# Performance work log

Measured on AMD Instinct MI355X. Metric: run time of the kernel, lower is better.

The kernel has to match this reference:

```python
import jax, jax.numpy as jnp
import numpy as np

B, N1, N2, D = 8, 2048, 2048, 512


def setup_inputs() -> dict:
    key = jax.random.key(0)
    k1, k2, k3 = jax.random.split(key, 3)
    matrix_1 = jax.random.normal(k1, (B, N1, D), dtype=jnp.float32)
    matrix_2 = jax.random.normal(k2, (B, N2, D), dtype=jnp.float32)
    # Linear similarity with combination 'x,y': weight over concat([x, y]) -> size 2*D
    weight = jax.random.normal(k3, (2 * D,), dtype=jnp.float32) * (1.0 / np.sqrt(2 * D))
    bias = jnp.zeros((1,), dtype=jnp.float32)
    return {"matrix_1": matrix_1, "matrix_2": matrix_2, "weight": weight, "bias": bias}


def reference(matrix_1, matrix_2, weight, bias):
    # Faithful to MatrixAttention + default Linear similarity:
    # sim[b,i,j] = dot(weight, concat(matrix_1[b,i], matrix_2[b,j])) + bias
    # The original tiles both matrices to (B, N1, N2, D); mathematically this
    # factors into two projections plus a broadcast add (same math, no tiling).
    d = matrix_1.shape[-1]
    w1, w2 = weight[:d], weight[d:]
    s1 = jnp.einsum('bnd,d->bn', matrix_1, w1)  # (B, N1)
    s2 = jnp.einsum('bmd,d->bm', matrix_2, w2)  # (B, N2)
    return s1[:, :, None] + s2[:, None, :] + bias[0]  # (B, N1, N2)
```

## Files before the change

kernel.cpp:

```cpp
#include <hip/hip_runtime.h>


#define DDIM 512
#define BB   8
#define NN   2048
#define ROWS_PER_MAT (BB * NN)

__global__ __launch_bounds__(256) void dot_kernel(const float* __restrict__ m1,
                                                  const float* __restrict__ m2,
                                                  const float* __restrict__ w,
                                                  float* __restrict__ s) {
    int wave = (int)((blockIdx.x * blockDim.x + threadIdx.x) >> 6);
    int lane = threadIdx.x & 63;

    const float* src;
    const float* wp;
    int row;
    if (wave < ROWS_PER_MAT) {
        src = m1; wp = w;        row = wave;
    } else {
        src = m2; wp = w + DDIM; row = wave - ROWS_PER_MAT;
    }

    const float4* rp = reinterpret_cast<const float4*>(src + (size_t)row * DDIM);
    const float4* wv = reinterpret_cast<const float4*>(wp);

    float4 a0 = rp[lane];
    float4 b0 = wv[lane];
    float4 a1 = rp[lane + 64];
    float4 b1 = wv[lane + 64];

    float acc = a0.x * b0.x + a0.y * b0.y + a0.z * b0.z + a0.w * b0.w
              + a1.x * b1.x + a1.y * b1.y + a1.z * b1.z + a1.w * b1.w;

    #pragma unroll
    for (int off = 32; off > 0; off >>= 1)
        acc += __shfl_down(acc, off, 64);

    if (lane == 0) s[wave] = acc;
}

__global__ __launch_bounds__(256) void add_kernel(const float* __restrict__ s1,
                                                  const float* __restrict__ s2,
                                                  const float* __restrict__ bias,
                                                  float4* __restrict__ out) {
    const size_t total4 = (size_t)BB * NN * (NN / 4);
    const float bval = bias[0];
    const float4* s2v = reinterpret_cast<const float4*>(s2);

    for (size_t i = (size_t)blockIdx.x * blockDim.x + threadIdx.x;
         i < total4;
         i += (size_t)gridDim.x * blockDim.x) {
        int m4    = (int)(i & (NN / 4 - 1));
        size_t t  = i >> 9;
        int n     = (int)(t & (NN - 1));
        int b     = (int)(t >> 11);

        float v1 = s1[b * NN + n] + bval;
        float4 v2 = s2v[b * (NN / 4) + m4];
        out[i] = make_float4(v2.x + v1, v2.y + v1, v2.z + v1, v2.w + v1);
    }
}

extern "C" void kernel_launch(void* const* d_in, const int* in_sizes, int n_in,
                              void* d_out, int out_size, void* d_ws, size_t ws_size,
                              hipStream_t stream) {
    const float* m1   = (const float*)d_in[0];
    const float* m2   = (const float*)d_in[1];
    const float* w    = (const float*)d_in[2];
    const float* bias = (const float*)d_in[3];
    float* out = (float*)d_out;

    float* s  = (float*)d_ws;
    float* s1 = s;
    float* s2 = s + ROWS_PER_MAT;

    dot_kernel<<<(2 * ROWS_PER_MAT) / 4, 256, 0, stream>>>(m1, m2, w, s);

    add_kernel<<<2048, 256, 0, stream>>>(s1, s2, bias, (float4*)out);
}
```

Before: 37.77 us.

## Fuse matrix_1 projection into broadcast-add kernel and use nontemporal loads/stores

The first kernel now projects only matrix_2 into the workspace. A new fused kernel has each wave compute one matrix_1 row projection and then write that row's full 2048-wide output line directly from s2. This removes the separate s1 workspace round trip and the grid-stride add kernel's per-element index math. Nontemporal loads for the input rows and nontemporal stores for the output are meant to keep the large streamed data from polluting cache. The trade-off is that each fused wave serializes its dot product before a long store loop, which could reduce memory-level parallelism.

```diff
diff --git a/kernel.cpp b/kernel.cpp
--- a/kernel.cpp
+++ b/kernel.cpp
@@ -4,61 +4,58 @@
 #define DDIM 512
 #define BB   8
 #define NN   2048
-#define ROWS_PER_MAT (BB * NN)
+#define ROWS (BB * NN)
 
-__global__ __launch_bounds__(256) void dot_kernel(const float* __restrict__ m1,
-                                                  const float* __restrict__ m2,
-                                                  const float* __restrict__ w,
-                                                  float* __restrict__ s) {
+typedef float f32x4 __attribute__((ext_vector_type(4)));
+
+__device__ __forceinline__ float dot_row_wave(const f32x4* __restrict__ rp,
+                                              const f32x4* __restrict__ wv,
+                                              int lane) {
+    f32x4 a0 = __builtin_nontemporal_load(rp + lane);
+    f32x4 b0 = wv[lane];
+    f32x4 a1 = __builtin_nontemporal_load(rp + lane + 64);
+    f32x4 b1 = wv[lane + 64];
+    float acc = a0.x * b0.x + a0.y * b0.y + a0.z * b0.z + a0.w * b0.w
+              + a1.x * b1.x + a1.y * b1.y + a1.z * b1.z + a1.w * b1.w;
+    #pragma unroll
+    for (int off = 1; off < 64; off <<= 1)
+        acc += __shfl_xor(acc, off, 64);
+    return acc;
+}
+
+__global__ __launch_bounds__(256) void dot2_kernel(const float* __restrict__ m2,
+                                                   const float* __restrict__ w,
+                                                   float* __restrict__ s2) {
     int wave = (int)((blockIdx.x * blockDim.x + threadIdx.x) >> 6);
     int lane = threadIdx.x & 63;
+    const f32x4* rp = reinterpret_cast<const f32x4*>(m2 + (size_t)wave * DDIM);
+    const f32x4* wv = reinterpret_cast<const f32x4*>(w + DDIM);
+    float acc = dot_row_wave(rp, wv, lane);
+    if (lane == 0) s2[wave] = acc;
+}
 
-    const float* src;
-    const float* wp;
-    int row;
-    if (wave < ROWS_PER_MAT) {
-        src = m1; wp = w;        row = wave;
-    } else {
-        src = m2; wp = w + DDIM; row = wave - ROWS_PER_MAT;
-    }
+__global__ __launch_bounds__(256) void fused_kernel(const float* __restrict__ m1,
+                                                    const float* __restrict__ w,
+                                                    const float* __restrict__ s2,
+                                                    const float* __restrict__ bias,
+                                                    float* __restrict__ out) {
+    int wave = (int)((blockIdx.x * blockDim.x + threadIdx.x) >> 6);
+    int lane = threadIdx.x & 63;
+    int b = wave >> 11;
 
-    const float4* rp = reinterpret_cast<const float4*>(src + (size_t)row * DDIM);
-    const float4* wv = reinterpret_cast<const float4*>(wp);
+    const f32x4* rp = reinterpret_cast<const f32x4*>(m1 + (size_t)wave * DDIM);
+    const f32x4* wv = reinterpret_cast<const f32x4*>(w);
+    float s1 = dot_row_wave(rp, wv, lane);
+    float v1 = s1 + bias[0];
 
-    float4 a0 = rp[lane];
-    float4 b0 = wv[lane];
-    float4 a1 = rp[lane + 64];
-    float4 b1 = wv[lane + 64];
-
-    float acc = a0.x * b0.x + a0.y * b0.y + a0.z * b0.z + a0.w * b0.w
-              + a1.x * b1.x + a1.y * b1.y + a1.z * b1.z + a1.w * b1.w;
+    const f32x4* s2v = reinterpret_cast<const f32x4*>(s2 + (size_t)b * NN);
+    f32x4* op = reinterpret_cast<f32x4*>(out + (size_t)wave * NN);
 
     #pragma unroll
-    for (int off = 32; off > 0; off >>= 1)
-        acc += __shfl_down(acc, off, 64);
-
-    if (lane == 0) s[wave] = acc;
-}
-
-__global__ __launch_bounds__(256) void add_kernel(const float* __restrict__ s1,
-                                                  const float* __restrict__ s2,
-                                                  const float* __restrict__ bias,
-                                                  float4* __restrict__ out) {
-    const size_t total4 = (size_t)BB * NN * (NN / 4);
-    const float bval = bias[0];
-    const float4* s2v = reinterpret_cast<const float4*>(s2);
-
-    for (size_t i = (size_t)blockIdx.x * blockDim.x + threadIdx.x;
-         i < total4;
-         i += (size_t)gridDim.x * blockDim.x) {
-        int m4    = (int)(i & (NN / 4 - 1));
-        size_t t  = i >> 9;
-        int n     = (int)(t & (NN - 1));
-        int b     = (int)(t >> 11);
-
-        float v1 = s1[b * NN + n] + bval;
-        float4 v2 = s2v[b * (NN / 4) + m4];
-        out[i] = make_float4(v2.x + v1, v2.y + v1, v2.z + v1, v2.w + v1);
+    for (int k = 0; k < 8; ++k) {
+        f32x4 v2 = s2v[lane + 64 * k];
+        f32x4 r  = v2 + v1;
+        __builtin_nontemporal_store(r, op + lane + 64 * k);
     }
 }
 
@@ -70,12 +67,8 @@
     const float* w    = (const float*)d_in[2];
     const float* bias = (const float*)d_in[3];
     float* out = (float*)d_out;
+    float* s2  = (float*)d_ws;
 
-    float* s  = (float*)d_ws;
-    float* s1 = s;
-    float* s2 = s + ROWS_PER_MAT;
-
-    dot_kernel<<<(2 * ROWS_PER_MAT) / 4, 256, 0, stream>>>(m1, m2, w, s);
-
-    add_kernel<<<2048, 256, 0, stream>>>(s1, s2, bias, (float4*)out);
+    dot2_kernel<<<ROWS / 4, 256, 0, stream>>>(m2, w, s2);
+    fused_kernel<<<ROWS / 4, 256, 0, stream>>>(m1, w, s2, bias, out);
 }
```

Result: slower. 41.81 us (+10.7%).
